# Performance work log

Hardware: AMD Instinct MI355X
Metric: run time of the kernel (lower is better)

Reference implementation:

```python
import jax, jax.numpy as jnp
import numpy as np

N_NODES = 50000
N_EDGES = 1600000
D = 128
LEAKY_SLOPE = 0.01  # torch nn.LeakyReLU default


def setup_inputs() -> dict:
    key = jax.random.key(0)
    ks = jax.random.split(key, 7)
    entity_embed = jax.random.normal(ks[0], (N_NODES, D), dtype=jnp.float32)
    W1 = jax.random.normal(ks[1], (D, D), dtype=jnp.float32) * 0.05
    b1 = jax.random.normal(ks[2], (D,), dtype=jnp.float32) * 0.05
    W2 = jax.random.normal(ks[3], (D, D), dtype=jnp.float32) * 0.05
    b2 = jax.random.normal(ks[4], (D,), dtype=jnp.float32) * 0.05
    src = jax.random.randint(ks[5], (N_EDGES,), 0, N_NODES, dtype=jnp.int32)
    dst = jax.random.randint(ks[6], (N_EDGES,), 0, N_NODES, dtype=jnp.int32)
    return {"entity_embed": entity_embed, "W1": W1, "b1": b1,
            "W2": W2, "b2": b2, "src": src, "dst": dst}


def reference(entity_embed, W1, b1, W2, b2, src, dst):
    # DGL update_all(copy_u('node','side'), sum('side','H')):
    # H[v] = sum over edges (u -> v) of entity_embed[u]
    n = entity_embed.shape[0]
    H = jax.ops.segment_sum(entity_embed[src], dst, num_segments=n)  # [N, D]
    # neighbors branch: LeakyReLU(W_1 @ H)
    neighbors = jax.nn.leaky_relu(H @ W1.T + b1, negative_slope=LEAKY_SLOPE)
    # interactions branch: LeakyReLU(W_2 @ (node * H))
    interactions = jax.nn.leaky_relu((entity_embed * H) @ W2.T + b2,
                                     negative_slope=LEAKY_SLOPE)
    # dropout is identity at inference
    return neighbors + interactions
```

## Files before the change

### kernel.cpp

```cpp
#include <hip/hip_runtime.h>

#define NN 50000
#define DD 128
#define SLOPE 0.01f
#define NB 782
#define BCAP 2560
#define ECH 6144
#define BST 512
#define PB 2
#define OVCAP 8192
#define HP 136

using bf16x8 = __attribute__((ext_vector_type(8))) short;
using f32x4  = __attribute__((ext_vector_type(4))) float;

__device__ inline float bflo(unsigned int w) { return __uint_as_float(w << 16); }
__device__ inline float bfhi(unsigned int w) { return __uint_as_float(w & 0xffff0000u); }
__device__ inline float sbf(short s) {
    return __uint_as_float(((unsigned int)(unsigned short)s) << 16);
}
__device__ inline unsigned int rnebf(float f) {
    unsigned int u = __float_as_uint(f);
    return (u + 0x7fffu + ((u >> 16) & 1u)) >> 16;
}
__device__ inline unsigned int pack2(float lo, float hi) {
    return rnebf(lo) | (rnebf(hi) << 16);
}
__device__ inline uint4 pack8f(const float* f) {
    uint4 o;
    o.x = pack2(f[0], f[1]); o.y = pack2(f[2], f[3]);
    o.z = pack2(f[4], f[5]); o.w = pack2(f[6], f[7]);
    return o;
}
__device__ inline void addrow(float* acc, uint4 r) {
    acc[0] += bflo(r.x); acc[1] += bfhi(r.x);
    acc[2] += bflo(r.y); acc[3] += bfhi(r.y);
    acc[4] += bflo(r.z); acc[5] += bfhi(r.z);
    acc[6] += bflo(r.w); acc[7] += bfhi(r.w);
}

__global__ __launch_bounds__(256) void convert_bf(
    const float* __restrict__ E, const float* __restrict__ W1,
    const float* __restrict__ W2, unsigned short* __restrict__ Ebf,
    unsigned short* __restrict__ W1b, unsigned short* __restrict__ W2b)
{
    const int NE8 = NN * DD / 8;
    const int NW8 = DD * DD / 8;
    int t = blockIdx.x * 256 + threadIdx.x;
    const float* s; unsigned short* d; int idx;
    if (t < NE8)                { s = E;  d = Ebf; idx = t; }
    else if (t < NE8 + NW8)     { s = W1; d = W1b; idx = t - NE8; }
    else if (t < NE8 + 2 * NW8) { s = W2; d = W2b; idx = t - NE8 - NW8; }
    else return;
    float4 a = ((const float4*)s)[(size_t)idx * 2];
    float4 b = ((const float4*)s)[(size_t)idx * 2 + 1];
    uint4 o;
    o.x = pack2(a.x, a.y); o.y = pack2(a.z, a.w);
    o.z = pack2(b.x, b.y); o.w = pack2(b.z, b.w);
    ((uint4*)d)[idx] = o;
}

__global__ __launch_bounds__(BST) void bin_edges(
    const int* __restrict__ src, const int* __restrict__ dst,
    int* __restrict__ gtail, unsigned int* __restrict__ stag,
    int* __restrict__ ovf_cnt, int2* __restrict__ ovf,
    int n_edges)
{
    __shared__ unsigned int srt[ECH];
    __shared__ int cnt[NB], off[NB], pos[NB], gbase[NB];
    __shared__ int wsum[BST / 64];

    const int tid = threadIdx.x;
    const int e0 = blockIdx.x * ECH;
    const int m = min(ECH, n_edges - e0);

    for (int b = tid; b < NB; b += BST) cnt[b] = 0;
    __syncthreads();

    for (int i = tid; i < m; i += BST)
        atomicAdd(&cnt[dst[e0 + i] >> 6], 1);
    __syncthreads();

    const int lane = tid & 63, w = tid >> 6;
    int b0 = tid * PB;
    int loc[PB]; int s = 0;
    #pragma unroll
    for (int j = 0; j < PB; ++j) {
        int bb = b0 + j;
        int cv = (bb < NB) ? cnt[bb] : 0;
        loc[j] = s; s += cv;
    }
    int incl = s;
    #pragma unroll
    for (int d = 1; d < 64; d <<= 1) {
        int t2 = __shfl_up(incl, d);
        if (lane >= d) incl += t2;
    }
    if (lane == 63) wsum[w] = incl;
    __syncthreads();
    int wbase = 0;
    for (int w2 = 0; w2 < w; ++w2) wbase += wsum[w2];
    int base = wbase + incl - s;
    #pragma unroll
    for (int j = 0; j < PB; ++j) {
        int bb = b0 + j;
        if (bb < NB) { off[bb] = base + loc[j]; pos[bb] = base + loc[j]; }
    }
    __syncthreads();

    for (int i = tid; i < m; i += BST) {
        int v = dst[e0 + i];
        int u = src[e0 + i];
        int bb = v >> 6;
        int p = atomicAdd(&pos[bb], 1);
        srt[p] = (unsigned int)u | ((unsigned int)(v & 63) << 16)
               | ((unsigned int)bb << 22);
    }
    __syncthreads();

    for (int bb = tid; bb < NB; bb += BST) {
        int c = cnt[bb];
        if (c) gbase[bb] = atomicAdd(&gtail[bb], c);
    }
    __syncthreads();

    for (int i = tid; i < m; i += BST) {
        unsigned int r = srt[i];
        int bb = (int)(r >> 22);
        int gp = gbase[bb] + (i - off[bb]);
        if (gp < BCAP) {
            stag[(size_t)bb * BCAP + gp] = r & 0x3fffffu;
        } else {
            int oi = atomicAdd(ovf_cnt, 1);
            if (oi < OVCAP)
                ovf[oi] = make_int2((int)(r & 0xffffu),
                                    bb * 64 + (int)((r >> 16) & 63));
        }
    }
}

__global__ __launch_bounds__(256, 4) void bucket_fused(
    const unsigned short* __restrict__ Ebf, const int* __restrict__ gtail,
    const unsigned int* __restrict__ stag, const int* __restrict__ ovf_cnt,
    const int2* __restrict__ ovf,
    const unsigned short* __restrict__ W1b, const unsigned short* __restrict__ W2b,
    const float* __restrict__ b1, const float* __restrict__ b2,
    float* __restrict__ out)
{
    __shared__ unsigned short sorted[BCAP];
    __shared__ unsigned short Hs[64][HP];
    __shared__ int cnt[64], off[65], pos[64];
    __shared__ int s_novf;

    const int b = blockIdx.x;
    const int tid = threadIdx.x;
    int len = gtail[b]; len = len < BCAP ? len : BCAP;
    const unsigned int* seg = stag + (size_t)b * BCAP;

    if (tid == 0) { int t = *ovf_cnt; s_novf = t < OVCAP ? t : OVCAP; }
    if (tid < 64) cnt[tid] = 0;
    __syncthreads();
    for (int i = tid; i < len; i += 256)
        atomicAdd(&cnt[(seg[i] >> 16) & 63], 1);
    __syncthreads();
    if (tid < 64) {
        int cv = cnt[tid];
        int incl = cv;
        #pragma unroll
        for (int d = 1; d < 64; d <<= 1) {
            int t2 = __shfl_up(incl, d);
            if (tid >= d) incl += t2;
        }
        off[tid] = incl - cv;
        pos[tid] = incl - cv;
        if (tid == 63) off[64] = incl;
    }
    __syncthreads();
    for (int i = tid; i < len; i += 256) {
        unsigned int r = seg[i];
        int p = atomicAdd(&pos[(r >> 16) & 63], 1);
        sorted[p] = (unsigned short)(r & 0xffffu);
    }
    __syncthreads();
    const int novf = s_novf;

    const int g = tid >> 4;
    const int c = tid & 15;
    const uint4* E4 = (const uint4*)Ebf;
    for (int p4 = 0; p4 < 4; ++p4) {
        int nl = p4 * 16 + g;
        int v = b * 64 + nl;
        if (v >= NN) continue;
        float acc[8] = {};
        int i = off[nl], e1 = off[nl + 1];
        uint4 r[8];
        for (; i + 8 <= e1; i += 8) {
            #pragma unroll
            for (int k = 0; k < 8; ++k)
                r[k] = E4[(size_t)sorted[i + k] * 16 + c];
            __builtin_amdgcn_sched_barrier(0);
            #pragma unroll
            for (int k = 0; k < 8; ++k) addrow(acc, r[k]);
        }
        for (; i + 2 <= e1; i += 2) {
            uint4 r0 = E4[(size_t)sorted[i]     * 16 + c];
            uint4 r1 = E4[(size_t)sorted[i + 1] * 16 + c];
            addrow(acc, r0); addrow(acc, r1);
        }
        if (i < e1) addrow(acc, E4[(size_t)sorted[i] * 16 + c]);

        if (novf > 0) {
            for (int k = 0; k < novf; ++k) {
                int2 e = ovf[k];
                if (e.y == v) addrow(acc, E4[(size_t)e.x * 16 + c]);
            }
        }
        *(uint4*)&Hs[nl][c * 8] = pack8f(acc);
    }
    __syncthreads();

    const int wave = tid >> 6;
    const int lane = tid & 63;
    const int v0 = b * 64 + wave * 16;
    if (v0 >= NN) return;
    const int m = lane & 15;
    const int quad = lane >> 4;

    bf16x8 aH[4], aE[4];
    const unsigned short* hrow = &Hs[wave * 16 + m][quad * 8];
    const unsigned short* erow = Ebf + (size_t)(v0 + m) * DD + quad * 8;
    #pragma unroll
    for (int ks = 0; ks < 4; ++ks) {
        bf16x8 h8 = *(const bf16x8*)(hrow + ks * 32);
        bf16x8 e8 = *(const bf16x8*)(erow + ks * 32);
        aH[ks] = h8;
        bf16x8 eh;
        #pragma unroll
        for (int j = 0; j < 8; ++j)
            eh[j] = (short)rnebf(sbf(h8[j]) * sbf(e8[j]));
        aE[ks] = eh;
    }

    #pragma unroll
    for (int jt = 0; jt < 8; ++jt) {
        const int j0 = jt * 16;
        const unsigned short* w1r = W1b + (size_t)(j0 + m) * DD + quad * 8;
        const unsigned short* w2r = W2b + (size_t)(j0 + m) * DD + quad * 8;
        f32x4 acc1 = {0.f, 0.f, 0.f, 0.f}, acc2 = {0.f, 0.f, 0.f, 0.f};
        #pragma unroll
        for (int ks = 0; ks < 4; ++ks) {
            bf16x8 bw1 = *(const bf16x8*)(w1r + ks * 32);
            bf16x8 bw2 = *(const bf16x8*)(w2r + ks * 32);
            acc1 = __builtin_amdgcn_mfma_f32_16x16x32_bf16(aH[ks], bw1, acc1, 0, 0, 0);
            acc2 = __builtin_amdgcn_mfma_f32_16x16x32_bf16(aE[ks], bw2, acc2, 0, 0, 0);
        }
        const float bb1 = b1[j0 + m], bb2 = b2[j0 + m];
        #pragma unroll
        for (int i = 0; i < 4; ++i) {
            int row = v0 + quad * 4 + i;
            if (row < NN) {
                float x1 = acc1[i] + bb1; x1 = x1 > 0.f ? x1 : SLOPE * x1;
                float x2 = acc2[i] + bb2; x2 = x2 > 0.f ? x2 : SLOPE * x2;
                out[(size_t)row * DD + j0 + m] = x1 + x2;
            }
        }
    }
}

__global__ __launch_bounds__(256) void scatter_add(
    const float* __restrict__ E, const int* __restrict__ src,
    const int* __restrict__ dst, float* __restrict__ H, int n_edges)
{
    int t = blockIdx.x * 256 + threadIdx.x;
    int e = t >> 5;
    if (e >= n_edges) return;
    int c = t & 31;
    float4 a = ((const float4*)E)[(size_t)src[e] * 32 + c];
    float* hp = H + (size_t)dst[e] * DD + c * 4;
    atomicAdd(hp + 0, a.x); atomicAdd(hp + 1, a.y);
    atomicAdd(hp + 2, a.z); atomicAdd(hp + 3, a.w);
}

__global__ __launch_bounds__(256) void fused_mlp(
    const float* __restrict__ E, const float* __restrict__ H,
    const float* __restrict__ W1, const float* __restrict__ b1,
    const float* __restrict__ W2, const float* __restrict__ b2,
    float* __restrict__ out)
{
    __shared__ float Hsf[32][DD];
    __shared__ float EHs[32][DD];
    __shared__ float W1s[DD][20];
    __shared__ float W2s[DD][20];
    const int tid = threadIdx.x;
    const int v0 = blockIdx.x * 32;
    const int nvalid = min(32, NN - v0);
    for (int i = 0; i < 4; ++i) {
        int f = tid + 256 * i;
        int n = f >> 5, c = f & 31;
        float4 h = make_float4(0.f, 0.f, 0.f, 0.f);
        float4 eh = h;
        if (n < nvalid) {
            h = ((const float4*)H)[(size_t)(v0 + n) * 32 + c];
            float4 e4 = ((const float4*)E)[(size_t)(v0 + n) * 32 + c];
            eh = make_float4(e4.x * h.x, e4.y * h.y, e4.z * h.z, e4.w * h.w);
        }
        *((float4*)&Hsf[n][c * 4]) = h;
        *((float4*)&EHs[n][c * 4]) = eh;
    }
    const int jg = tid & 63;
    const int n0 = (tid >> 6) * 8;
    float acc1a[8] = {}, acc1b[8] = {}, acc2a[8] = {}, acc2b[8] = {};
    for (int t8 = 0; t8 < 8; ++t8) {
        const int k0 = t8 * 16;
        __syncthreads();
        for (int i = 0; i < 8; ++i) {
            int f = tid + 256 * i;
            int j = f >> 4, kk = f & 15;
            W1s[j][kk] = W1[j * DD + k0 + kk];
            W2s[j][kk] = W2[j * DD + k0 + kk];
        }
        __syncthreads();
        for (int c = 0; c < 4; ++c) {
            float4 w1a = *((const float4*)&W1s[jg][c * 4]);
            float4 w1b = *((const float4*)&W1s[jg + 64][c * 4]);
            float4 w2a = *((const float4*)&W2s[jg][c * 4]);
            float4 w2b = *((const float4*)&W2s[jg + 64][c * 4]);
            const int kk = k0 + c * 4;
            for (int n = 0; n < 8; ++n) {
                float4 h = *((const float4*)&Hsf[n0 + n][kk]);
                float4 eh = *((const float4*)&EHs[n0 + n][kk]);
                acc1a[n] += h.x * w1a.x + h.y * w1a.y + h.z * w1a.z + h.w * w1a.w;
                acc1b[n] += h.x * w1b.x + h.y * w1b.y + h.z * w1b.z + h.w * w1b.w;
                acc2a[n] += eh.x * w2a.x + eh.y * w2a.y + eh.z * w2a.z + eh.w * w2a.w;
                acc2b[n] += eh.x * w2b.x + eh.y * w2b.y + eh.z * w2b.z + eh.w * w2b.w;
            }
        }
    }
    const float b1a = b1[jg], b1b = b1[jg + 64];
    const float b2a = b2[jg], b2b = b2[jg + 64];
    for (int n = 0; n < 8; ++n) {
        if (n0 + n < nvalid) {
            const int v = v0 + n0 + n;
            float x1 = acc1a[n] + b1a; x1 = x1 > 0.f ? x1 : SLOPE * x1;
            float x2 = acc2a[n] + b2a; x2 = x2 > 0.f ? x2 : SLOPE * x2;
            out[(size_t)v * DD + jg] = x1 + x2;
            float y1 = acc1b[n] + b1b; y1 = y1 > 0.f ? y1 : SLOPE * y1;
            float y2 = acc2b[n] + b2b; y2 = y2 > 0.f ? y2 : SLOPE * y2;
            out[(size_t)v * DD + jg + 64] = y1 + y2;
        }
    }
}

extern "C" void kernel_launch(void* const* d_in, const int* in_sizes, int n_in,
                              void* d_out, int out_size, void* d_ws, size_t ws_size,
                              hipStream_t stream)
{
    const float* E  = (const float*)d_in[0];
    const float* W1 = (const float*)d_in[1];
    const float* b1 = (const float*)d_in[2];
    const float* W2 = (const float*)d_in[3];
    const float* b2 = (const float*)d_in[4];
    const int* src  = (const int*)d_in[5];
    const int* dst  = (const int*)d_in[6];
    float* out = (float*)d_out;
    const int n_edges = in_sizes[5];

    char* ws = (char*)d_ws;
    auto al = [](size_t x) { return (x + 255) & ~(size_t)255; };

    const size_t off_tail = 0;
    const size_t off_ovfc = (size_t)NB * 4;
    const size_t off_ovf  = al(off_ovfc + 4);
    const size_t off_stag = al(off_ovf + (size_t)OVCAP * 8);
    const size_t off_Ebf  = al(off_stag + (size_t)NB * BCAP * 4);
    const size_t off_W1b  = al(off_Ebf + (size_t)NN * DD * 2);
    const size_t off_W2b  = al(off_W1b + (size_t)DD * DD * 2);
    const size_t need_bf  = off_W2b + (size_t)DD * DD * 2;

    if (ws_size >= need_bf) {
        int*  gtail   = (int*)(ws + off_tail);
        int*  ovf_cnt = (int*)(ws + off_ovfc);
        int2* ovf     = (int2*)(ws + off_ovf);
        unsigned int*   stag = (unsigned int*)(ws + off_stag);
        unsigned short* Ebf  = (unsigned short*)(ws + off_Ebf);
        unsigned short* W1b  = (unsigned short*)(ws + off_W1b);
        unsigned short* W2b  = (unsigned short*)(ws + off_W2b);

        const int nbin = (n_edges + ECH - 1) / ECH;
        const int ncv  = NN * DD / 8 + 2 * (DD * DD / 8);
        const int ncvb = (ncv + 255) / 256;

        hipMemsetAsync(ws, 0, off_ovf, stream);
        convert_bf<<<ncvb, 256, 0, stream>>>(E, W1, W2, Ebf, W1b, W2b);
        bin_edges<<<nbin, BST, 0, stream>>>(
            src, dst, gtail, stag, ovf_cnt, ovf, n_edges);
        bucket_fused<<<NB, 256, 0, stream>>>(
            Ebf, gtail, stag, ovf_cnt, ovf, W1b, W2b, b1, b2, out);
        return;
    }

    const size_t hbytes = (size_t)NN * DD * sizeof(float);
    float* H = (ws_size >= hbytes) ? (float*)ws : out;
    hipMemsetAsync(H, 0, hbytes, stream);
    scatter_add<<<((n_edges * 32) + 255) / 256, 256, 0, stream>>>(
        E, src, dst, H, n_edges);
    fused_mlp<<<(NN + 31) / 32, 256, 0, stream>>>(E, H, W1, b1, W2, b2, out);
}
```

Measured before the change: 191.5 us.

## Replace atomic bucket tails with deterministic count-scan-scatter pipeline

Edge binning now runs as three steps: a per-chunk histogram pass fused into the bf16 conversion launch, a per-bucket exclusive scan over chunks, and a scatter pass that reads precomputed offsets. This removes the global atomicAdd on bucket tails and the memset, and gives a deterministic edge order. The cost is reading dst twice, an extra kernel launch and a counts matrix in the workspace. The gather loop in the fused kernel also widens its unroll from 8 to 16 loads, with a 4-wide remainder loop.

```diff
diff --git a/kernel.cpp b/kernel.cpp
--- a/kernel.cpp
+++ b/kernel.cpp
@@ -39,32 +39,76 @@
     acc[6] += bflo(r.w); acc[7] += bfhi(r.w);
 }
 
-__global__ __launch_bounds__(256) void convert_bf(
+__global__ __launch_bounds__(BST) void count_convert(
     const float* __restrict__ E, const float* __restrict__ W1,
-    const float* __restrict__ W2, unsigned short* __restrict__ Ebf,
-    unsigned short* __restrict__ W1b, unsigned short* __restrict__ W2b)
-{
-    const int NE8 = NN * DD / 8;
-    const int NW8 = DD * DD / 8;
-    int t = blockIdx.x * 256 + threadIdx.x;
-    const float* s; unsigned short* d; int idx;
-    if (t < NE8)                { s = E;  d = Ebf; idx = t; }
-    else if (t < NE8 + NW8)     { s = W1; d = W1b; idx = t - NE8; }
-    else if (t < NE8 + 2 * NW8) { s = W2; d = W2b; idx = t - NE8 - NW8; }
-    else return;
-    float4 a = ((const float4*)s)[(size_t)idx * 2];
-    float4 b = ((const float4*)s)[(size_t)idx * 2 + 1];
-    uint4 o;
-    o.x = pack2(a.x, a.y); o.y = pack2(a.z, a.w);
-    o.z = pack2(b.x, b.y); o.w = pack2(b.z, b.w);
-    ((uint4*)d)[idx] = o;
-}
-
-__global__ __launch_bounds__(BST) void bin_edges(
+    const float* __restrict__ W2, const int* __restrict__ dst,
+    unsigned short* __restrict__ Ebf, unsigned short* __restrict__ W1b,
+    unsigned short* __restrict__ W2b, int* __restrict__ cnt_g,
+    int n_edges, int nbin)
+{
+    const int tid = threadIdx.x;
+
+    if (blockIdx.x >= nbin) {
+        const int NE8 = NN * DD / 8;
+        const int NW8 = DD * DD / 8;
+        int t = (blockIdx.x - nbin) * BST + tid;
+        const float* s; unsigned short* d; int idx;
+        if (t < NE8)                { s = E;  d = Ebf; idx = t; }
+        else if (t < NE8 + NW8)     { s = W1; d = W1b; idx = t - NE8; }
+        else if (t < NE8 + 2 * NW8) { s = W2; d = W2b; idx = t - NE8 - NW8; }
+        else return;
+        float4 a = ((const float4*)s)[(size_t)idx * 2];
+        float4 b = ((const float4*)s)[(size_t)idx * 2 + 1];
+        uint4 o;
+        o.x = pack2(a.x, a.y); o.y = pack2(a.z, a.w);
+        o.z = pack2(b.x, b.y); o.w = pack2(b.z, b.w);
+        ((uint4*)d)[idx] = o;
+        return;
+    }
+
+    __shared__ int cnt[NB];
+    const int e0 = blockIdx.x * ECH;
+    const int m = min(ECH, n_edges - e0);
+
+    for (int b = tid; b < NB; b += BST) cnt[b] = 0;
+    __syncthreads();
+    for (int i = tid; i < m; i += BST)
+        atomicAdd(&cnt[dst[e0 + i] >> 6], 1);
+    __syncthreads();
+    for (int b = tid; b < NB; b += BST)
+        cnt_g[(size_t)b * nbin + blockIdx.x] = cnt[b];
+}
+
+__global__ __launch_bounds__(256) void scan_counts(
+    int* __restrict__ cnt_g, int* __restrict__ gtail,
+    int* __restrict__ ovf_cnt, int nbin)
+{
+    if (blockIdx.x == 0 && threadIdx.x == 0) *ovf_cnt = 0;
+    const int w = threadIdx.x >> 6, lane = threadIdx.x & 63;
+    const int bb = blockIdx.x * 4 + w;
+    if (bb >= NB) return;
+    int* row = cnt_g + (size_t)bb * nbin;
+    int carry = 0;
+    for (int base = 0; base < nbin; base += 64) {
+        int blk = base + lane;
+        int v = (blk < nbin) ? row[blk] : 0;
+        int incl = v;
+        #pragma unroll
+        for (int d = 1; d < 64; d <<= 1) {
+            int t = __shfl_up(incl, d);
+            if (lane >= d) incl += t;
+        }
+        if (blk < nbin) row[blk] = carry + incl - v;
+        carry += __shfl(incl, 63);
+    }
+    if (lane == 0) gtail[bb] = carry;
+}
+
+__global__ __launch_bounds__(BST) void scatter_edges(
     const int* __restrict__ src, const int* __restrict__ dst,
-    int* __restrict__ gtail, unsigned int* __restrict__ stag,
+    const int* __restrict__ cnt_g, unsigned int* __restrict__ stag,
     int* __restrict__ ovf_cnt, int2* __restrict__ ovf,
-    int n_edges)
+    int n_edges, int nbin)
 {
     __shared__ unsigned int srt[ECH];
     __shared__ int cnt[NB], off[NB], pos[NB], gbase[NB];
@@ -79,6 +123,8 @@
 
     for (int i = tid; i < m; i += BST)
         atomicAdd(&cnt[dst[e0 + i] >> 6], 1);
+    for (int b = tid; b < NB; b += BST)
+        gbase[b] = cnt_g[(size_t)b * nbin + blockIdx.x];
     __syncthreads();
 
     const int lane = tid & 63, w = tid >> 6;
@@ -115,12 +161,6 @@
         int p = atomicAdd(&pos[bb], 1);
         srt[p] = (unsigned int)u | ((unsigned int)(v & 63) << 16)
                | ((unsigned int)bb << 22);
-    }
-    __syncthreads();
-
-    for (int bb = tid; bb < NB; bb += BST) {
-        int c = cnt[bb];
-        if (c) gbase[bb] = atomicAdd(&gtail[bb], c);
     }
     __syncthreads();
 
@@ -193,21 +233,24 @@
         if (v >= NN) continue;
         float acc[8] = {};
         int i = off[nl], e1 = off[nl + 1];
-        uint4 r[8];
-        for (; i + 8 <= e1; i += 8) {
+        uint4 r[16];
+        for (; i + 16 <= e1; i += 16) {
             #pragma unroll
-            for (int k = 0; k < 8; ++k)
+            for (int k = 0; k < 16; ++k)
                 r[k] = E4[(size_t)sorted[i + k] * 16 + c];
             __builtin_amdgcn_sched_barrier(0);
             #pragma unroll
-            for (int k = 0; k < 8; ++k) addrow(acc, r[k]);
-        }
-        for (; i + 2 <= e1; i += 2) {
-            uint4 r0 = E4[(size_t)sorted[i]     * 16 + c];
-            uint4 r1 = E4[(size_t)sorted[i + 1] * 16 + c];
-            addrow(acc, r0); addrow(acc, r1);
-        }
-        if (i < e1) addrow(acc, E4[(size_t)sorted[i] * 16 + c]);
+            for (int k = 0; k < 16; ++k) addrow(acc, r[k]);
+        }
+        for (; i + 4 <= e1; i += 4) {
+            #pragma unroll
+            for (int k = 0; k < 4; ++k)
+                r[k] = E4[(size_t)sorted[i + k] * 16 + c];
+            __builtin_amdgcn_sched_barrier(0);
+            #pragma unroll
+            for (int k = 0; k < 4; ++k) addrow(acc, r[k]);
+        }
+        for (; i < e1; ++i) addrow(acc, E4[(size_t)sorted[i] * 16 + c]);
 
         if (novf > 0) {
             for (int k = 0; k < novf; ++k) {
@@ -368,6 +411,8 @@
     char* ws = (char*)d_ws;
     auto al = [](size_t x) { return (x + 255) & ~(size_t)255; };
 
+    const int nbin = (n_edges + ECH - 1) / ECH;
+
     const size_t off_tail = 0;
     const size_t off_ovfc = (size_t)NB * 4;
     const size_t off_ovf  = al(off_ovfc + 4);
@@ -375,7 +420,8 @@
     const size_t off_Ebf  = al(off_stag + (size_t)NB * BCAP * 4);
     const size_t off_W1b  = al(off_Ebf + (size_t)NN * DD * 2);
     const size_t off_W2b  = al(off_W1b + (size_t)DD * DD * 2);
-    const size_t need_bf  = off_W2b + (size_t)DD * DD * 2;
+    const size_t off_cntg = al(off_W2b + (size_t)DD * DD * 2);
+    const size_t need_bf  = off_cntg + (size_t)NB * nbin * 4;
 
     if (ws_size >= need_bf) {
         int*  gtail   = (int*)(ws + off_tail);
@@ -385,15 +431,17 @@
         unsigned short* Ebf  = (unsigned short*)(ws + off_Ebf);
         unsigned short* W1b  = (unsigned short*)(ws + off_W1b);
         unsigned short* W2b  = (unsigned short*)(ws + off_W2b);
-
-        const int nbin = (n_edges + ECH - 1) / ECH;
+        int*  cnt_g   = (int*)(ws + off_cntg);
+
         const int ncv  = NN * DD / 8 + 2 * (DD * DD / 8);
-        const int ncvb = (ncv + 255) / 256;
-
-        hipMemsetAsync(ws, 0, off_ovf, stream);
-        convert_bf<<<ncvb, 256, 0, stream>>>(E, W1, W2, Ebf, W1b, W2b);
-        bin_edges<<<nbin, BST, 0, stream>>>(
-            src, dst, gtail, stag, ovf_cnt, ovf, n_edges);
+        const int ncvb = (ncv + BST - 1) / BST;
+
+        count_convert<<<nbin + ncvb, BST, 0, stream>>>(
+            E, W1, W2, dst, Ebf, W1b, W2b, cnt_g, n_edges, nbin);
+        scan_counts<<<(NB + 3) / 4, 256, 0, stream>>>(
+            cnt_g, gtail, ovf_cnt, nbin);
+        scatter_edges<<<nbin, BST, 0, stream>>>(
+            src, dst, cnt_g, stag, ovf_cnt, ovf, n_edges, nbin);
         bucket_fused<<<NB, 256, 0, stream>>>(
             Ebf, gtail, stag, ovf_cnt, ovf, W1b, W2b, b1, b2, out);
         return;
```

New measurement: 196.8 us. +2.8%, slower.

## Replace single-pass edge binning with two-level radix bucketing fused with bf16 conversion

Applied to the files above, without the earlier changes.

Edge binning now runs as a coarse 49-way scatter into superbuckets, followed by a rebin kernel that splits each superbucket into 16 final 64-node buckets. This replaces the 782-bin shared-memory sort and scan per chunk. The coarse scatter is merged into the same launch as the bf16 conversion of E and the weights, removing one kernel launch and letting the two pieces of work overlap. The gather loop is unrolled to 16 in-flight loads. The cost is an extra pass of writes and reads over the staged edges, more global atomics, and higher register pressure in the gather.

```diff
diff --git a/kernel.cpp b/kernel.cpp
--- a/kernel.cpp
+++ b/kernel.cpp
@@ -4,10 +4,13 @@
 #define DD 128
 #define SLOPE 0.01f
 #define NB 782
-#define BCAP 2560
-#define ECH 6144
-#define BST 512
-#define PB 2
+#define BCAP 2304
+#define NSB 49
+#define SBW 1024
+#define SCAP 34816
+#define ECH1 4096
+#define RSL 2048
+#define RS 17
 #define OVCAP 8192
 #define HP 136
 
@@ -25,12 +28,6 @@
 }
 __device__ inline unsigned int pack2(float lo, float hi) {
     return rnebf(lo) | (rnebf(hi) << 16);
-}
-__device__ inline uint4 pack8f(const float* f) {
-    uint4 o;
-    o.x = pack2(f[0], f[1]); o.y = pack2(f[2], f[3]);
-    o.z = pack2(f[4], f[5]); o.w = pack2(f[6], f[7]);
-    return o;
 }
 __device__ inline void addrow(float* acc, uint4 r) {
     acc[0] += bflo(r.x); acc[1] += bfhi(r.x);
@@ -39,14 +36,13 @@
     acc[6] += bflo(r.w); acc[7] += bfhi(r.w);
 }
 
-__global__ __launch_bounds__(256) void convert_bf(
+__device__ inline void convert_item(
     const float* __restrict__ E, const float* __restrict__ W1,
     const float* __restrict__ W2, unsigned short* __restrict__ Ebf,
-    unsigned short* __restrict__ W1b, unsigned short* __restrict__ W2b)
+    unsigned short* __restrict__ W1b, unsigned short* __restrict__ W2b, int t)
 {
     const int NE8 = NN * DD / 8;
     const int NW8 = DD * DD / 8;
-    int t = blockIdx.x * 256 + threadIdx.x;
     const float* s; unsigned short* d; int idx;
     if (t < NE8)                { s = E;  d = Ebf; idx = t; }
     else if (t < NE8 + NW8)     { s = W1; d = W1b; idx = t - NE8; }
@@ -60,81 +56,102 @@
     ((uint4*)d)[idx] = o;
 }
 
-__global__ __launch_bounds__(BST) void bin_edges(
-    const int* __restrict__ src, const int* __restrict__ dst,
+__global__ __launch_bounds__(512) void scatter_convert(
+    const float* __restrict__ E, const float* __restrict__ W1,
+    const float* __restrict__ W2, const int* __restrict__ src,
+    const int* __restrict__ dst, unsigned short* __restrict__ Ebf,
+    unsigned short* __restrict__ W1b, unsigned short* __restrict__ W2b,
+    int* __restrict__ gtail1, unsigned int* __restrict__ stag1,
+    int* __restrict__ ovf_cnt, int2* __restrict__ ovf,
+    int n_edges, int nch1)
+{
+    const int tid = threadIdx.x;
+    if (blockIdx.x >= nch1) {
+        convert_item(E, W1, W2, Ebf, W1b, W2b,
+                     (blockIdx.x - nch1) * 512 + tid);
+        return;
+    }
+
+    __shared__ int cnt49[NSB];
+    const int e0 = blockIdx.x * ECH1;
+    int vv[8], uu[8];
+
+    if (tid < NSB) cnt49[tid] = 0;
+    __syncthreads();
+    #pragma unroll
+    for (int k = 0; k < 8; ++k) {
+        int idx = e0 + tid + k * 512;
+        if (idx < n_edges) {
+            vv[k] = dst[idx]; uu[k] = src[idx];
+            atomicAdd(&cnt49[vv[k] >> 10], 1);
+        } else vv[k] = -1;
+    }
+    __syncthreads();
+    if (tid < NSB) {
+        int c = cnt49[tid];
+        cnt49[tid] = c ? atomicAdd(&gtail1[tid], c) : 0;
+    }
+    __syncthreads();
+    #pragma unroll
+    for (int k = 0; k < 8; ++k) {
+        if (vv[k] < 0) continue;
+        int sb = vv[k] >> 10;
+        int p = atomicAdd(&cnt49[sb], 1);
+        if (p < SCAP) {
+            stag1[(size_t)sb * SCAP + p] =
+                (unsigned int)uu[k] | ((unsigned int)(vv[k] & 1023) << 16);
+        } else {
+            int oi = atomicAdd(ovf_cnt, 1);
+            if (oi < OVCAP) ovf[oi] = make_int2(uu[k], vv[k]);
+        }
+    }
+}
+
+__global__ __launch_bounds__(256) void rebin(
+    const int* __restrict__ gtail1, const unsigned int* __restrict__ stag1,
     int* __restrict__ gtail, unsigned int* __restrict__ stag,
-    int* __restrict__ ovf_cnt, int2* __restrict__ ovf,
-    int n_edges)
-{
-    __shared__ unsigned int srt[ECH];
-    __shared__ int cnt[NB], off[NB], pos[NB], gbase[NB];
-    __shared__ int wsum[BST / 64];
-
+    int* __restrict__ ovf_cnt, int2* __restrict__ ovf)
+{
+    const int sb = blockIdx.x / RS, sl = blockIdx.x % RS;
     const int tid = threadIdx.x;
-    const int e0 = blockIdx.x * ECH;
-    const int m = min(ECH, n_edges - e0);
-
-    for (int b = tid; b < NB; b += BST) cnt[b] = 0;
-    __syncthreads();
-
-    for (int i = tid; i < m; i += BST)
-        atomicAdd(&cnt[dst[e0 + i] >> 6], 1);
-    __syncthreads();
-
-    const int lane = tid & 63, w = tid >> 6;
-    int b0 = tid * PB;
-    int loc[PB]; int s = 0;
-    #pragma unroll
-    for (int j = 0; j < PB; ++j) {
-        int bb = b0 + j;
-        int cv = (bb < NB) ? cnt[bb] : 0;
-        loc[j] = s; s += cv;
-    }
-    int incl = s;
-    #pragma unroll
-    for (int d = 1; d < 64; d <<= 1) {
-        int t2 = __shfl_up(incl, d);
-        if (lane >= d) incl += t2;
-    }
-    if (lane == 63) wsum[w] = incl;
-    __syncthreads();
-    int wbase = 0;
-    for (int w2 = 0; w2 < w; ++w2) wbase += wsum[w2];
-    int base = wbase + incl - s;
-    #pragma unroll
-    for (int j = 0; j < PB; ++j) {
-        int bb = b0 + j;
-        if (bb < NB) { off[bb] = base + loc[j]; pos[bb] = base + loc[j]; }
-    }
-    __syncthreads();
-
-    for (int i = tid; i < m; i += BST) {
-        int v = dst[e0 + i];
-        int u = src[e0 + i];
-        int bb = v >> 6;
-        int p = atomicAdd(&pos[bb], 1);
-        srt[p] = (unsigned int)u | ((unsigned int)(v & 63) << 16)
-               | ((unsigned int)bb << 22);
-    }
-    __syncthreads();
-
-    for (int bb = tid; bb < NB; bb += BST) {
-        int c = cnt[bb];
-        if (c) gbase[bb] = atomicAdd(&gtail[bb], c);
-    }
-    __syncthreads();
-
-    for (int i = tid; i < m; i += BST) {
-        unsigned int r = srt[i];
-        int bb = (int)(r >> 22);
-        int gp = gbase[bb] + (i - off[bb]);
-        if (gp < BCAP) {
-            stag[(size_t)bb * BCAP + gp] = r & 0x3fffffu;
+    int len = gtail1[sb]; len = len < SCAP ? len : SCAP;
+    const int i0 = sl * RSL;
+    const int i1 = min(i0 + RSL, len);
+
+    __shared__ int cnt16[16], pos16[16];
+    if (tid < 16) cnt16[tid] = 0;
+    __syncthreads();
+
+    unsigned int r[8];
+    const unsigned int* seg = stag1 + (size_t)sb * SCAP;
+    #pragma unroll
+    for (int k = 0; k < 8; ++k) {
+        int idx = i0 + tid + k * 256;
+        if (idx < i1) {
+            r[k] = seg[idx];
+            atomicAdd(&cnt16[(r[k] >> 22) & 15], 1);
+        } else r[k] = 0xffffffffu;
+    }
+    __syncthreads();
+    if (tid < 16) {
+        int c = cnt16[tid];
+        int bb = sb * 16 + tid;
+        pos16[tid] = (c && bb < NB) ? atomicAdd(&gtail[bb], c) : 0;
+    }
+    __syncthreads();
+    #pragma unroll
+    for (int k = 0; k < 8; ++k) {
+        if (r[k] == 0xffffffffu) continue;
+        int j = (r[k] >> 22) & 15;
+        int p = atomicAdd(&pos16[j], 1);
+        int bb = sb * 16 + j;
+        if (p < BCAP) {
+            stag[(size_t)bb * BCAP + p] = r[k] & 0x3fffffu;
         } else {
             int oi = atomicAdd(ovf_cnt, 1);
             if (oi < OVCAP)
-                ovf[oi] = make_int2((int)(r & 0xffffu),
-                                    bb * 64 + (int)((r >> 16) & 63));
+                ovf[oi] = make_int2((int)(r[k] & 0xffffu),
+                                    sb * SBW + (int)((r[k] >> 16) & 1023));
         }
     }
 }
@@ -193,21 +210,24 @@
         if (v >= NN) continue;
         float acc[8] = {};
         int i = off[nl], e1 = off[nl + 1];
-        uint4 r[8];
-        for (; i + 8 <= e1; i += 8) {
+        uint4 r[16];
+        for (; i + 16 <= e1; i += 16) {
             #pragma unroll
-            for (int k = 0; k < 8; ++k)
+            for (int k = 0; k < 16; ++k)
                 r[k] = E4[(size_t)sorted[i + k] * 16 + c];
             __builtin_amdgcn_sched_barrier(0);
             #pragma unroll
-            for (int k = 0; k < 8; ++k) addrow(acc, r[k]);
-        }
-        for (; i + 2 <= e1; i += 2) {
-            uint4 r0 = E4[(size_t)sorted[i]     * 16 + c];
-            uint4 r1 = E4[(size_t)sorted[i + 1] * 16 + c];
-            addrow(acc, r0); addrow(acc, r1);
-        }
-        if (i < e1) addrow(acc, E4[(size_t)sorted[i] * 16 + c]);
+            for (int k = 0; k < 16; ++k) addrow(acc, r[k]);
+        }
+        for (; i + 4 <= e1; i += 4) {
+            #pragma unroll
+            for (int k = 0; k < 4; ++k)
+                r[k] = E4[(size_t)sorted[i + k] * 16 + c];
+            __builtin_amdgcn_sched_barrier(0);
+            #pragma unroll
+            for (int k = 0; k < 4; ++k) addrow(acc, r[k]);
+        }
+        for (; i < e1; ++i) addrow(acc, E4[(size_t)sorted[i] * 16 + c]);
 
         if (novf > 0) {
             for (int k = 0; k < novf; ++k) {
@@ -215,7 +235,10 @@
                 if (e.y == v) addrow(acc, E4[(size_t)e.x * 16 + c]);
             }
         }
-        *(uint4*)&Hs[nl][c * 8] = pack8f(acc);
+        uint4 o;
+        o.x = pack2(acc[0], acc[1]); o.y = pack2(acc[2], acc[3]);
+        o.z = pack2(acc[4], acc[5]); o.w = pack2(acc[6], acc[7]);
+        *(uint4*)&Hs[nl][c * 8] = o;
     }
     __syncthreads();
 
@@ -368,32 +391,37 @@
     char* ws = (char*)d_ws;
     auto al = [](size_t x) { return (x + 255) & ~(size_t)255; };
 
-    const size_t off_tail = 0;
-    const size_t off_ovfc = (size_t)NB * 4;
-    const size_t off_ovf  = al(off_ovfc + 4);
-    const size_t off_stag = al(off_ovf + (size_t)OVCAP * 8);
-    const size_t off_Ebf  = al(off_stag + (size_t)NB * BCAP * 4);
-    const size_t off_W1b  = al(off_Ebf + (size_t)NN * DD * 2);
-    const size_t off_W2b  = al(off_W1b + (size_t)DD * DD * 2);
-    const size_t need_bf  = off_W2b + (size_t)DD * DD * 2;
+    const int nch1 = (n_edges + ECH1 - 1) / ECH1;
+
+    const size_t ctr_ints  = NSB + 1 + NB;
+    const size_t off_ovf   = al(ctr_ints * 4);
+    const size_t off_stag1 = al(off_ovf + (size_t)OVCAP * 8);
+    const size_t off_stag  = al(off_stag1 + (size_t)NSB * SCAP * 4);
+    const size_t off_Ebf   = al(off_stag + (size_t)NB * BCAP * 4);
+    const size_t off_W1b   = al(off_Ebf + (size_t)NN * DD * 2);
+    const size_t off_W2b   = al(off_W1b + (size_t)DD * DD * 2);
+    const size_t need_bf   = off_W2b + (size_t)DD * DD * 2;
 
     if (ws_size >= need_bf) {
-        int*  gtail   = (int*)(ws + off_tail);
-        int*  ovf_cnt = (int*)(ws + off_ovfc);
+        int*  gtail1  = (int*)ws;
+        int*  ovf_cnt = gtail1 + NSB;
+        int*  gtail   = gtail1 + NSB + 1;
         int2* ovf     = (int2*)(ws + off_ovf);
-        unsigned int*   stag = (unsigned int*)(ws + off_stag);
-        unsigned short* Ebf  = (unsigned short*)(ws + off_Ebf);
-        unsigned short* W1b  = (unsigned short*)(ws + off_W1b);
-        unsigned short* W2b  = (unsigned short*)(ws + off_W2b);
-
-        const int nbin = (n_edges + ECH - 1) / ECH;
-        const int ncv  = NN * DD / 8 + 2 * (DD * DD / 8);
-        const int ncvb = (ncv + 255) / 256;
-
-        hipMemsetAsync(ws, 0, off_ovf, stream);
-        convert_bf<<<ncvb, 256, 0, stream>>>(E, W1, W2, Ebf, W1b, W2b);
-        bin_edges<<<nbin, BST, 0, stream>>>(
-            src, dst, gtail, stag, ovf_cnt, ovf, n_edges);
+        unsigned int*   stag1 = (unsigned int*)(ws + off_stag1);
+        unsigned int*   stag  = (unsigned int*)(ws + off_stag);
+        unsigned short* Ebf   = (unsigned short*)(ws + off_Ebf);
+        unsigned short* W1b   = (unsigned short*)(ws + off_W1b);
+        unsigned short* W2b   = (unsigned short*)(ws + off_W2b);
+
+        const int NCV  = NN * DD / 8 + 2 * (DD * DD / 8);
+        const int ncvb = (NCV + 511) / 512;
+
+        hipMemsetAsync(ws, 0, ctr_ints * 4, stream);
+        scatter_convert<<<nch1 + ncvb, 512, 0, stream>>>(
+            E, W1, W2, src, dst, Ebf, W1b, W2b,
+            gtail1, stag1, ovf_cnt, ovf, n_edges, nch1);
+        rebin<<<NSB * RS, 256, 0, stream>>>(
+            gtail1, stag1, gtail, stag, ovf_cnt, ovf);
         bucket_fused<<<NB, 256, 0, stream>>>(
             Ebf, gtail, stag, ovf_cnt, ovf, W1b, W2b, b1, b2, out);
         return;
```

Result: slower. 195.8 us (+2.3%).
